# Kernel optimization log

Measured on AMD Instinct MI355X. Metric: run time of the kernel, lower is better.

The kernel has to match this reference:

```python
import jax, jax.numpy as jnp
import numpy as np

MAX_SEGMENTS = 196
BN_EPS = 1e-5

def _conv(x, w, pad, dil=1):
    return jax.lax.conv_general_dilated(
        x, w, window_strides=(1, 1), padding=[(pad, pad), (pad, pad)],
        rhs_dilation=(dil, dil), dimension_numbers=('NCHW', 'OIHW', 'NCHW'))

def _bn(x, g, b, m, v):
    inv = g / jnp.sqrt(v + BN_EPS)
    return x * inv[None, :, None, None] + (b - m * inv)[None, :, None, None]

def setup_inputs() -> dict:
    key = jax.random.key(0)
    ks = jax.random.split(key, 20)
    B, H, W = 2, 224, 224
    E = 768
    inp = {
        'img': jax.random.normal(ks[0], (B, 3, H, W), jnp.float32),
        'segments': jax.random.randint(ks[1], (B, H, W), 0, MAX_SEGMENTS, jnp.int32),
        'centroids': jax.random.uniform(ks[2], (B, MAX_SEGMENTS, 2), jnp.float32) * 223.0,
        'conv1_w': jax.random.normal(ks[3], (64, 3, 3, 3), jnp.float32) * 0.1,
        'conv1_b': jax.random.normal(ks[4], (64,), jnp.float32) * 0.1,
        'bn1_g': jax.random.uniform(ks[5], (64,), jnp.float32) + 0.5,
        'bn1_b': jax.random.normal(ks[6], (64,), jnp.float32) * 0.1,
        'bn1_m': jax.random.normal(ks[7], (64,), jnp.float32) * 0.1,
        'bn1_v': jax.random.uniform(ks[8], (64,), jnp.float32) + 0.5,
        'conv2_w': jax.random.normal(ks[9], (E, 64, 3, 3), jnp.float32) * 0.05,
        'conv2_b': jax.random.normal(ks[10], (E,), jnp.float32) * 0.1,
        'bn2_g': jax.random.uniform(ks[11], (E,), jnp.float32) + 0.5,
        'bn2_b': jax.random.normal(ks[12], (E,), jnp.float32) * 0.1,
        'bn2_m': jax.random.normal(ks[13], (E,), jnp.float32) * 0.1,
        'bn2_v': jax.random.uniform(ks[14], (E,), jnp.float32) + 0.5,
        'edge_w': jax.random.normal(ks[15], (2, 1, 3, 3), jnp.float32) * 0.2,
        'pos_w': jax.random.normal(ks[16], (E, 2), jnp.float32) * 0.5,
        'pos_b': jax.random.normal(ks[17], (E,), jnp.float32) * 0.1,
        'fusion_w': jax.random.normal(ks[18], (E, 2 * E), jnp.float32) * 0.02,
        'fusion_b': jax.random.normal(ks[19], (E,), jnp.float32) * 0.1,
    }
    return inp

def reference(img, segments, centroids, conv1_w, conv1_b, bn1_g, bn1_b, bn1_m, bn1_v,
              conv2_w, conv2_b, bn2_g, bn2_b, bn2_m, bn2_v, edge_w,
              pos_w, pos_b, fusion_w, fusion_b):
    B, _, H, W = img.shape
    M = MAX_SEGMENTS
    # CNN feature extractor: [B, E, H, W]
    x = jax.nn.relu(_bn(_conv(img, conv1_w, pad=1) + conv1_b[None, :, None, None],
                        bn1_g, bn1_b, bn1_m, bn1_v))
    feats = jax.nn.relu(_bn(_conv(x, conv2_w, pad=2, dil=2) + conv2_b[None, :, None, None],
                            bn2_g, bn2_b, bn2_m, bn2_v))
    C = feats.shape[1]
    # Edge detection on grayscale
    gray = jnp.mean(img, axis=1, keepdims=True)
    edges = _conv(gray, edge_w, pad=1)  # [B, 2, H, W]
    gradient_map = jnp.sqrt(edges[:, 0] ** 2 + edges[:, 1] ** 2 + 1e-8)  # [B, H, W]
    similarity = jnp.clip(1.0 - gradient_map, 0.0, 1.0)
    # Global per-(batch, segment) ids
    ids = (jnp.arange(B, dtype=jnp.int32)[:, None] * M + segments.reshape(B, -1)).reshape(-1)
    K = B * M
    ones = jnp.ones((B * H * W,), jnp.float32)
    counts = jax.ops.segment_sum(ones, ids, num_segments=K)              # [K]
    n_K = jnp.maximum(counts, 1.0)
    sim_sum = jax.ops.segment_sum(similarity.reshape(-1), ids, num_segments=K)
    W_k = (sim_sum / n_K).reshape(B, M)
    # Segment mean / max pooling of features
    ff = feats.transpose(0, 2, 3, 1).reshape(-1, C)                      # [B*H*W, C]
    emb_mean = (jax.ops.segment_sum(ff, ids, num_segments=K) / n_K[:, None]).reshape(B, M, C)
    mx = jax.ops.segment_max(ff, ids, num_segments=K)
    emb_max = jnp.where(counts[:, None] > 0, mx, 0.0).reshape(B, M, C)   # empty segments -> 0
    concat = jnp.concatenate([emb_mean, emb_max], axis=-1)               # [B, M, 2C]
    fused = jnp.einsum('bmc,dc->bmd', concat, fusion_w) + fusion_b
    weighted = fused * W_k[:, :, None]
    # Positional embeddings from normalized centroids
    cn = jnp.stack([centroids[:, :, 0] / float(W), centroids[:, :, 1] / float(H)], axis=-1)
    pos = jnp.einsum('bmc,dc->bmd', cn, pos_w) + pos_b                   # n_centroids == M
    final_embeddings = weighted + pos
    return final_embeddings, gradient_map, segments
```

## Files before the change

### kernel.cpp

```cpp
#include <hip/hip_runtime.h>
#include <hip/hip_fp8.h>

#define B_ 2
#define H_ 224
#define W_ 224
#define HW_ 50176
#define E_ 768
#define M_ 196

typedef __attribute__((ext_vector_type(8))) short short8;
typedef __attribute__((ext_vector_type(4))) float floatx4;

__device__ __forceinline__ float bf2f(ushort u){ return __uint_as_float(((unsigned)u)<<16); }
__device__ __forceinline__ ushort f2bf(float f){
  unsigned b = __float_as_uint(f);
  b += 0x7fffu + ((b>>16)&1u);
  return (ushort)(b>>16);
}
__device__ __forceinline__ unsigned pack4_fp8(float a, float b, float c, float d){
  int v = __builtin_amdgcn_cvt_pk_fp8_f32(a, b, 0, false);
  v = __builtin_amdgcn_cvt_pk_fp8_f32(c, d, v, true);
  return (unsigned)v;
}

__device__ __forceinline__ void ld_g2l16(const void* g, void* l){
  __builtin_amdgcn_global_load_lds((const __attribute__((address_space(1))) unsigned int*)g,
                                   (__attribute__((address_space(3))) unsigned int*)l, 16, 0, 0);
}

__global__ void prep_edge_k(const float* __restrict__ w2, const float* __restrict__ cb2,
                            const float* __restrict__ g2, const float* __restrict__ be2,
                            const float* __restrict__ mn2, const float* __restrict__ vr2,
                            ushort* __restrict__ wt2, float* __restrict__ bias2,
                            const float* __restrict__ w1, const float* __restrict__ cb1,
                            const float* __restrict__ g1, const float* __restrict__ be1,
                            const float* __restrict__ mn1, const float* __restrict__ vr1,
                            ushort* __restrict__ wA, float* __restrict__ bias1,
                            const float* __restrict__ img, const int* __restrict__ seg,
                            const float* __restrict__ ew, float* __restrict__ out,
                            float* __restrict__ counts, float* __restrict__ sims,
                            int* __restrict__ scnt){
  __shared__ ushort WT[9216];
  __shared__ float aux[196];
  __shared__ float aux2[196];
  int tid = threadIdx.x;
  if (blockIdx.x < 48){
    int co0 = blockIdx.x * 16;
    if (tid < 16){
      float inv = g2[co0+tid] * rsqrtf(vr2[co0+tid] + 1e-5f);
      aux[tid] = inv;
      bias2[co0+tid] = cb2[co0+tid]*inv + be2[co0+tid] - mn2[co0+tid]*inv;
    }
    __syncthreads();
    #pragma unroll
    for (int j = 0; j < 36; j++){
      int idx = j*256 + tid;
      WT[idx] = f2bf(w2[(size_t)co0*576 + idx] * aux[idx/576]);
    }
    __syncthreads();
    #pragma unroll
    for (int j = 0; j < 5; j++){
      int o = j*256 + tid;
      if (o < 1152){
        int tapkc = o >> 4, col = o & 15;
        int tap = tapkc >> 3, kc = tapkc & 7;
        ushort tmp[8];
        #pragma unroll
        for (int e=0; e<8; e++)
          tmp[e] = WT[col*576 + (kc*8+e)*9 + tap];
        *reinterpret_cast<uint4*>(&wt2[(size_t)((tap*8 + kc)*768 + co0 + col)*8]) =
            *reinterpret_cast<const uint4*>(tmp);
      }
    }
    return;
  }
  if (blockIdx.x == 48){
    #pragma unroll
    for (int j = 0; j < 8; j++){
      int t = j*256 + tid;
      int co = t >> 5, k = t & 31;
      float inv = g1[co] * rsqrtf(vr1[co] + 1e-5f);
      float val = 0.f;
      if (k < 27){
        int tap = k / 3, ci = k % 3;
        val = w1[co*27 + ci*9 + tap] * inv;
      }
      wA[co*32 + k] = f2bf(val);
      if (k == 0) bias1[co] = cb1[co]*inv + be1[co] - mn1[co]*inv;
    }
    return;
  }
  if (tid < 196){ aux[tid]=0.f; aux2[tid]=0.f; }
  __syncthreads();
  int p = (blockIdx.x-49)*256 + tid;
  int b = p / HW_; int r = p % HW_; int h = r / W_; int w = r % W_;
  float e0=0.f, e1=0.f;
  #pragma unroll
  for (int ky=0;ky<3;ky++){
    int hh=h+ky-1;
    #pragma unroll
    for (int kx=0;kx<3;kx++){
      int ww=w+kx-1;
      float gv=0.f;
      if (hh>=0&&hh<H_&&ww>=0&&ww<W_){
        int base = b*3*HW_ + hh*W_ + ww;
        gv=(img[base]+img[base+HW_]+img[base+2*HW_])*(1.f/3.f);
      }
      e0 += gv*ew[ky*3+kx];
      e1 += gv*ew[9+ky*3+kx];
    }
  }
  float gm = sqrtf(e0*e0+e1*e1+1e-8f);
  out[301056 + p] = gm;
  int sg = seg[p];
  out[401408 + p] = (float)sg;
  float sim = fminf(fmaxf(1.f-gm,0.f),1.f);
  atomicAdd(&aux[sg], 1.f);
  atomicAdd(&aux2[sg], sim);
  __syncthreads();
  if (tid < 196){
    int gid = b*196 + tid;
    float c = aux[tid];
    atomicAdd(&counts[gid], c);
    atomicAdd(&sims[gid], aux2[tid]);
    atomicAdd(&scnt[b*196+tid], (int)c);
  }
}

__launch_bounds__(256)
__global__ void conv1_scan_k(const float* __restrict__ img, const ushort* __restrict__ wA,
                             const float* __restrict__ bias1, ushort* __restrict__ xbf,
                             const int* __restrict__ scnt, int* __restrict__ offs,
                             int* __restrict__ curs){
  __shared__ float HL[3*18*20];
  __shared__ ushort IC[256*40];
  __shared__ ushort AW[64*40];
  __shared__ float b1s[64];
  int tid = threadIdx.x;
  if (blockIdx.x < 2){
    int* a = reinterpret_cast<int*>(HL);
    int s = blockIdx.x;
    a[tid] = (tid<196)? scnt[s*196+tid] : 0;
    __syncthreads();
    for (int d=1; d<256; d<<=1){
      int v = a[tid];
      int u = (tid>=d)? a[tid-d] : 0;
      __syncthreads();
      a[tid] = v+u;
      __syncthreads();
    }
    if (tid<=196) offs[s*200+tid] = tid ? a[tid-1] : 0;
    if (tid<196)  curs[s*196+tid] = tid ? a[tid-1] : 0;
    return;
  }
  int bid = blockIdx.x - 2;
  int b = bid / 196, tile = bid % 196;
  int tr = tile / 14, tc = tile % 14;
  int h0 = tr*16, w0 = tc*16;
  for (int idx = tid; idx < 972; idx += 256){
    int ci = idx / 324, rem = idx % 324;
    int r = rem / 18, c = rem % 18;
    int hh = h0 + r - 1, ww = w0 + c - 1;
    float v = (hh>=0 && hh<H_ && ww>=0 && ww<W_) ? img[((b*3+ci)*H_+hh)*W_+ww] : 0.f;
    HL[ci*360 + r*20 + c] = v;
  }
  {
    int row = tid >> 2, cp = (tid&3)*8;
    uint4 v = *reinterpret_cast<const uint4*>(&wA[row*32 + cp]);
    *reinterpret_cast<uint4*>(&AW[row*40 + cp]) = v;
  }
  if (tid < 64) b1s[tid] = bias1[tid];
  __syncthreads();
  {
    int pr = tid >> 4, pc = tid & 15;
    ushort tmp[32];
    #pragma unroll
    for (int ky=0; ky<3; ky++)
      #pragma unroll
      for (int kx=0; kx<3; kx++)
        #pragma unroll
        for (int ci=0; ci<3; ci++)
          tmp[(ky*3+kx)*3+ci] = f2bf(HL[ci*360 + (pr+ky)*20 + (pc+kx)]);
    #pragma unroll
    for (int k=27; k<32; k++) tmp[k] = 0;
    #pragma unroll
    for (int j=0; j<4; j++)
      *reinterpret_cast<uint4*>(&IC[tid*40 + j*8]) = *reinterpret_cast<const uint4*>(&tmp[j*8]);
  }
  __syncthreads();
  int lane = tid & 63, wave = tid >> 6;
  int q = lane >> 4, l15 = lane & 15;
  short8 af[4], bfr[4];
  #pragma unroll
  for (int f=0; f<4; f++)
    af[f] = *reinterpret_cast<const short8*>(&AW[(f*16+l15)*40 + q*8]);
  #pragma unroll
  for (int f=0; f<4; f++)
    bfr[f] = *reinterpret_cast<const short8*>(&IC[(wave*64+f*16+l15)*40 + q*8]);
  floatx4 acc[4][4];
  #pragma unroll
  for (int fc=0; fc<4; fc++)
    #pragma unroll
    for (int fp=0; fp<4; fp++){
      floatx4 z = (floatx4){0.f,0.f,0.f,0.f};
      acc[fc][fp] = __builtin_amdgcn_mfma_f32_16x16x32_bf16(af[fc], bfr[fp], z, 0,0,0);
    }
  #pragma unroll
  for (int fp=0; fp<4; fp++){
    int pxl = wave*64 + fp*16 + l15;
    size_t gp = (size_t)b*HW_ + (size_t)(h0 + (pxl>>4))*W_ + (w0 + (pxl&15));
    #pragma unroll
    for (int fc=0; fc<4; fc++){
      int co4 = fc*16 + q*4;
      ushort o[4];
      #pragma unroll
      for (int r=0; r<4; r++) o[r] = f2bf(fmaxf(acc[fc][fp][r] + b1s[co4+r], 0.f));
      *reinterpret_cast<uint2*>(&xbf[gp*64 + co4]) = *reinterpret_cast<const uint2*>(o);
    }
  }
}

__launch_bounds__(256, 2)
__global__ void conv2_scatter_k(const ushort* __restrict__ xbf, const ushort* __restrict__ wt2,
                                const float* __restrict__ bias2, unsigned char* __restrict__ feats,
                                const int* __restrict__ seg, int* __restrict__ curs,
                                int* __restrict__ list){
  __shared__ ushort SM[25600 + 12288];
  ushort* XH = SM;
  ushort* WL = SM + 25600;
  int tid = threadIdx.x;
  if (blockIdx.y == 0){
    if (blockIdx.x < 392){
      int p = blockIdx.x*256 + tid;
      int b = p / HW_;
      int pos = atomicAdd(&curs[b*196+seg[p]], 1);
      list[b*HW_ + pos] = p;
    }
    return;
  }
  int lane = tid & 63, wave = tid >> 6;
  int wc = wave >> 1, wp = wave & 1;
  int q = lane >> 4, l15 = lane & 15;
  int bt = blockIdx.x / 196, tile = blockIdx.x % 196;
  int tr = tile / 14, tc = tile % 14;
  int co0 = (blockIdx.y - 1) * 128;
  int h0 = tr*16, w0 = tc*16;

  for (int px = tid; px < 400; px += 256){
    int hr = px / 20, wcol = px % 20;
    int hh = h0 + hr - 2, ww = w0 + wcol - 2;
    bool ok = (hh>=0 && hh<H_ && ww>=0 && ww<W_);
    const uint4* src = reinterpret_cast<const uint4*>(&xbf[(((size_t)bt*H_+hh)*W_+ww)*64]);
    #pragma unroll
    for (int chl=0; chl<8; chl++){
      uint4 val = ok ? src[chl] : make_uint4(0u,0u,0u,0u);
      *reinterpret_cast<uint4*>(&XH[chl*3200 + px*8]) = val;
    }
  }
  #pragma unroll
  for (int j=0;j<4;j++){
    int idx = tid + 256*j;
    int srci = ((idx>>7)*768 + co0 + (idx&127))*8;
    ld_g2l16(&wt2[srci], &WL[(idx & ~63)*8]);
  }
  __syncthreads();

  floatx4 acc[4][8];
  #pragma unroll
  for (int i=0;i<4;i++)
    #pragma unroll
    for (int j=0;j<8;j++) acc[i][j] = (floatx4){0.f,0.f,0.f,0.f};

  int wbase = q*1024 + (wc*64 + l15)*8;
  int xb    = q*3200 + wp*1280 + l15*8;

  #pragma unroll
  for (int hs = 0; hs < 18; hs++){
    if (hs == 17) { asm volatile("s_waitcnt vmcnt(0)" ::: "memory"); }
    else          { asm volatile("s_waitcnt vmcnt(2)" ::: "memory"); }
    __builtin_amdgcn_s_barrier();
    const int s0 = (2*hs) % 6;
    if (hs < 16){
      const int p0 = (2*hs + 4) % 6;
      #pragma unroll
      for (int j=0;j<2;j++){
        int idx = tid + 256*j;
        int srci = ((4*(hs+2) + (idx>>7))*768 + co0 + (idx&127))*8;
        ld_g2l16(&wt2[srci], &WL[p0*2048 + (idx & ~63)*8]);
      }
    }
    const int tap = hs >> 1, half = hs & 1;
    const int dyr = (tap/3)*2, dxr = (tap%3)*2;
    const int xoff = half*12800 + dyr*160 + dxr*8;
    short8 af[4], bx[8];
    #pragma unroll
    for (int f=0; f<4; f++)
      af[f] = *reinterpret_cast<const short8*>(&WL[s0*2048 + wbase + f*128]);
    #pragma unroll
    for (int fp=0; fp<8; fp++)
      bx[fp] = *reinterpret_cast<const short8*>(&XH[xb + xoff + fp*160]);
    __builtin_amdgcn_s_setprio(1);
    #pragma unroll
    for (int fc=0; fc<4; fc++)
      #pragma unroll
      for (int fp=0; fp<8; fp++)
        acc[fc][fp] = __builtin_amdgcn_mfma_f32_16x16x32_bf16(af[fc], bx[fp], acc[fc][fp], 0,0,0);
    __builtin_amdgcn_s_setprio(0);
  }

  __syncthreads();
  unsigned* EP = reinterpret_cast<unsigned*>(SM);
  #pragma unroll
  for (int fc=0; fc<4; fc++){
    float4 bs = *reinterpret_cast<const float4*>(&bias2[co0 + wc*64 + fc*16 + q*4]);
    int cslot = wc*16 + fc*4 + q;
    #pragma unroll
    for (int fp=0; fp<8; fp++){
      int p_local = (wp*8 + fp)*16 + l15;
      EP[p_local*33 + cslot] = pack4_fp8(
          fmaxf(acc[fc][fp][0] + bs.x, 0.f), fmaxf(acc[fc][fp][1] + bs.y, 0.f),
          fmaxf(acc[fc][fp][2] + bs.z, 0.f), fmaxf(acc[fc][fp][3] + bs.w, 0.f));
    }
  }
  __syncthreads();
  {
    size_t gbase = ((size_t)bt*HW_ + (size_t)(tr*16)*W_ + tc*16)*768 + co0;
    int c = tid & 31, t5 = tid >> 5;
    #pragma unroll
    for (int j=0; j<32; j++){
      int px = j*8 + t5;
      int rr = px >> 4, wcol = px & 15;
      *reinterpret_cast<unsigned*>(
        &feats[gbase + ((size_t)rr*W_ + wcol)*768 + c*4]) = EP[px*33 + c];
    }
  }
}

__global__ void pool_k(const unsigned char* __restrict__ feats, const int* __restrict__ list,
                       const int* __restrict__ offs, float* __restrict__ meansum,
                       float* __restrict__ maxv){
  int m = blockIdx.x, qu = blockIdx.y, b = blockIdx.z, tid = threadIdx.x;
  int base = offs[b*200+m], end = offs[b*200+m+1];
  int len = end - base;
  int b0 = base + ((len*qu) >> 3);
  int b1 = base + ((len*(qu+1)) >> 3);
  const int* lp = &list[b*HW_];
  int co4 = tid*4;
  float s0=0.f,s1=0.f,s2=0.f,s3=0.f;
  float m0=0.f,m1=0.f,m2=0.f,m3=0.f;
  int i = b0;
  #define ACC(v) { \
    float f0=__builtin_amdgcn_cvt_f32_fp8((int)(v),0), f1=__builtin_amdgcn_cvt_f32_fp8((int)(v),1); \
    float f2=__builtin_amdgcn_cvt_f32_fp8((int)(v),2), f3=__builtin_amdgcn_cvt_f32_fp8((int)(v),3); \
    s0+=f0; s1+=f1; s2+=f2; s3+=f3; \
    m0=fmaxf(m0,f0); m1=fmaxf(m1,f1); m2=fmaxf(m2,f2); m3=fmaxf(m3,f3); }
  for (; i+3 < b1; i += 4){
    unsigned va = *reinterpret_cast<const unsigned*>(&feats[(size_t)lp[i  ]*768 + co4]);
    unsigned vb = *reinterpret_cast<const unsigned*>(&feats[(size_t)lp[i+1]*768 + co4]);
    unsigned vc = *reinterpret_cast<const unsigned*>(&feats[(size_t)lp[i+2]*768 + co4]);
    unsigned vd = *reinterpret_cast<const unsigned*>(&feats[(size_t)lp[i+3]*768 + co4]);
    ACC(va) ACC(vb) ACC(vc) ACC(vd)
  }
  for (; i < b1; i++){
    unsigned v = *reinterpret_cast<const unsigned*>(&feats[(size_t)lp[i]*768 + co4]);
    ACC(v)
  }
  #undef ACC
  int gs = b*196 + m;
  float* ms = &meansum[(size_t)gs*768 + co4];
  unsigned* mv = reinterpret_cast<unsigned*>(&maxv[(size_t)gs*768 + co4]);
  atomicAdd(&ms[0], s0); atomicAdd(&ms[1], s1);
  atomicAdd(&ms[2], s2); atomicAdd(&ms[3], s3);
  atomicMax(&mv[0], __float_as_uint(m0)); atomicMax(&mv[1], __float_as_uint(m1));
  atomicMax(&mv[2], __float_as_uint(m2)); atomicMax(&mv[3], __float_as_uint(m3));
}

__launch_bounds__(256)
__global__ void fusion_mfma_k(const float* __restrict__ meansum, const float* __restrict__ maxv,
                              const float* __restrict__ counts, const float* __restrict__ fw,
                              float* __restrict__ partial){
  __shared__ ushort SM2[2*128*72];
  ushort* AL = SM2;
  ushort* BL = SM2 + 128*72;
  int tid = threadIdx.x;
  int lane = tid & 63, wave = tid >> 6;
  int wc = wave >> 1, wp = wave & 1;
  int q = lane >> 4, l15 = lane & 15;
  int co0 = blockIdx.x * 128;
  int m0  = blockIdx.y * 128;
  int ksz = blockIdx.z;
  floatx4 acc[4][4];
  for (int i=0;i<4;i++) for (int j=0;j<4;j++) acc[i][j] = (floatx4){0.f,0.f,0.f,0.f};

  for (int kb=0; kb<3; kb++){
    int k0 = ksz*192 + kb*64;
    __syncthreads();
    #pragma unroll
    for (int i=0;i<4;i++){
      int idx = tid + 256*i;
      int row = idx >> 3, c8 = (idx & 7) * 8;
      int gm = m0 + row;
      float4 a0 = make_float4(0.f,0.f,0.f,0.f), a1 = a0;
      if (gm < 392){
        int k = k0 + c8;
        if (k < 768){
          float invc = 1.f / fmaxf(counts[gm], 1.f);
          a0 = *reinterpret_cast<const float4*>(&meansum[gm*768 + k]);
          a1 = *reinterpret_cast<const float4*>(&meansum[gm*768 + k + 4]);
          a0.x*=invc; a0.y*=invc; a0.z*=invc; a0.w*=invc;
          a1.x*=invc; a1.y*=invc; a1.z*=invc; a1.w*=invc;
        } else {
          a0 = *reinterpret_cast<const float4*>(&maxv[gm*768 + k - 768]);
          a1 = *reinterpret_cast<const float4*>(&maxv[gm*768 + k - 768 + 4]);
        }
      }
      ushort ua[8] = { f2bf(a0.x),f2bf(a0.y),f2bf(a0.z),f2bf(a0.w),
                       f2bf(a1.x),f2bf(a1.y),f2bf(a1.z),f2bf(a1.w) };
      *reinterpret_cast<uint4*>(&AL[row*72 + c8]) = *reinterpret_cast<uint4*>(ua);
      float4 b0 = *reinterpret_cast<const float4*>(&fw[(co0+row)*1536 + k0 + c8]);
      float4 b1 = *reinterpret_cast<const float4*>(&fw[(co0+row)*1536 + k0 + c8 + 4]);
      ushort ub[8] = { f2bf(b0.x),f2bf(b0.y),f2bf(b0.z),f2bf(b0.w),
                       f2bf(b1.x),f2bf(b1.y),f2bf(b1.z),f2bf(b1.w) };
      *reinterpret_cast<uint4*>(&BL[row*72 + c8]) = *reinterpret_cast<uint4*>(ub);
    }
    __syncthreads();
    #pragma unroll
    for (int ks=0; ks<64; ks+=32){
      short8 af[4], bfr[4];
      #pragma unroll
      for (int f=0; f<4; f++)
        af[f] = *reinterpret_cast<const short8*>(&AL[(wc*64+f*16+l15)*72 + ks + q*8]);
      #pragma unroll
      for (int f=0; f<4; f++)
        bfr[f] = *reinterpret_cast<const short8*>(&BL[(wp*64+f*16+l15)*72 + ks + q*8]);
      #pragma unroll
      for (int fm=0; fm<4; fm++)
        #pragma unroll
        for (int fn=0; fn<4; fn++)
          acc[fm][fn] = __builtin_amdgcn_mfma_f32_16x16x32_bf16(af[fm], bfr[fn], acc[fm][fn], 0,0,0);
    }
  }
  float* pp = &partial[(size_t)ksz * 301056];
  #pragma unroll
  for (int fm=0; fm<4; fm++){
    #pragma unroll
    for (int r2=0; r2<4; r2++){
      int m = m0 + wc*64 + fm*16 + q*4 + r2;
      if (m >= 392) continue;
      #pragma unroll
      for (int fn=0; fn<4; fn++){
        int co = co0 + wp*64 + fn*16 + l15;
        pp[(size_t)m*768 + co] = acc[fm][fn][r2];
      }
    }
  }
}

__global__ void fuse_ep_k(const float* __restrict__ partial, const float* __restrict__ fb,
                          const float* __restrict__ sims, const float* __restrict__ counts,
                          const float* __restrict__ cent, const float* __restrict__ pw,
                          const float* __restrict__ pb, float* __restrict__ out){
  int t = blockIdx.x*256 + threadIdx.x;
  int gm = t / 768, co = t % 768;
  float s = 0.f;
  #pragma unroll
  for (int k=0;k<8;k++) s += partial[(size_t)k*301056 + t];
  float wk = sims[gm] / fmaxf(counts[gm], 1.f);
  float cx = cent[gm*2 + 0] * (1.f/224.f);
  float cy = cent[gm*2 + 1] * (1.f/224.f);
  out[t] = (s + fb[co]) * wk + cx*pw[co*2] + cy*pw[co*2+1] + pb[co];
}

extern "C" void kernel_launch(void* const* d_in, const int* in_sizes, int n_in,
                              void* d_out, int out_size, void* d_ws, size_t ws_size,
                              hipStream_t stream){
  const float* img  = (const float*)d_in[0];
  const int*   seg  = (const int*)  d_in[1];
  const float* cent = (const float*)d_in[2];
  const float* c1w  = (const float*)d_in[3];
  const float* c1b  = (const float*)d_in[4];
  const float* bn1g = (const float*)d_in[5];
  const float* bn1b = (const float*)d_in[6];
  const float* bn1m = (const float*)d_in[7];
  const float* bn1v = (const float*)d_in[8];
  const float* c2w  = (const float*)d_in[9];
  const float* c2b  = (const float*)d_in[10];
  const float* bn2g = (const float*)d_in[11];
  const float* bn2b = (const float*)d_in[12];
  const float* bn2m = (const float*)d_in[13];
  const float* bn2v = (const float*)d_in[14];
  const float* ew   = (const float*)d_in[15];
  const float* pw   = (const float*)d_in[16];
  const float* pb   = (const float*)d_in[17];
  const float* fwp  = (const float*)d_in[18];
  const float* fbp  = (const float*)d_in[19];
  float* out = (float*)d_out;
  char* ws = (char*)d_ws;

  ushort* xbf    = (ushort*)(ws + 0);
  ushort* wt2    = (ushort*)(ws + 12845056);
  float*  bias2  = (float*) (ws + 13729792);
  float*  meansum= (float*) (ws + 13732864);
  float*  maxv   = (float*) (ws + 14937088);
  float*  counts = (float*) (ws + 16141312);
  float*  sims   = (float*) (ws + 16142880);
  int*    scnt   = (int*)   (ws + 16144448);
  int*    offs   = (int*)   (ws + 16147584);
  int*    curs   = (int*)   (ws + 16150784);
  int*    list   = (int*)   (ws + 16154112);
  ushort* wA     = (ushort*)(ws + 16154112);
  float*  bias1  = (float*) (ws + 16158208);
  unsigned char* feats = (unsigned char*)(ws + 16555520);
  float*  partial= (float*) (ws + 16555520);

  (void)hipMemsetAsync(ws + 13732864, 0, 2414720, stream);
  prep_edge_k<<<441, 256, 0, stream>>>(c2w, c2b, bn2g, bn2b, bn2m, bn2v, wt2, bias2,
                                       c1w, c1b, bn1g, bn1b, bn1m, bn1v, wA, bias1,
                                       img, seg, ew, out, counts, sims, scnt);
  conv1_scan_k<<<394, 256, 0, stream>>>(img, wA, bias1, xbf, scnt, offs, curs);
  conv2_scatter_k<<<dim3(392, 7), 256, 0, stream>>>(xbf, wt2, bias2, feats, seg, curs, list);
  pool_k<<<dim3(196, 8, 2), 192, 0, stream>>>(feats, list, offs, meansum, maxv);
  fusion_mfma_k<<<dim3(6, 4, 8), 256, 0, stream>>>(meansum, maxv, counts, fwp, partial);
  fuse_ep_k<<<1176, 256, 0, stream>>>(partial, fbp, sims, counts, cent, pw, pb, out);
}
```

Measured before the change: 306.9 us.

## Double-buffer LDS fragment loads in conv2 MFMA loop and repad epilogue

Restructures the conv2 main loop so the A/B fragments for the next half-step are read from LDS into a second register set while the current MFMAs run. The weight ring changes from six slots to three slots of double size with vmcnt(0) waits. The epilogue staging stride changes from 33 to 34 words. The aim is to hide LDS read latency behind MFMA work, at the cost of doubling fragment registers (which may lower occupancy) and a stricter wait on global loads.

```diff
diff --git a/kernel.cpp b/kernel.cpp
--- a/kernel.cpp
+++ b/kernel.cpp
@@ -258,10 +258,13 @@
     }
   }
   #pragma unroll
-  for (int j=0;j<4;j++){
-    int idx = tid + 256*j;
-    int srci = ((idx>>7)*768 + co0 + (idx&127))*8;
-    ld_g2l16(&wt2[srci], &WL[(idx & ~63)*8]);
+  for (int k=0;k<2;k++){
+    #pragma unroll
+    for (int j=0;j<2;j++){
+      int idx = tid + 256*j;
+      int srci = ((4*k + (idx>>7))*768 + co0 + (idx&127))*8;
+      ld_g2l16(&wt2[srci], &WL[k*4096 + (idx & ~63)*8]);
+    }
   }
   __syncthreads();
 
@@ -271,40 +274,49 @@
     #pragma unroll
     for (int j=0;j<8;j++) acc[i][j] = (floatx4){0.f,0.f,0.f,0.f};
 
-  int wbase = q*1024 + (wc*64 + l15)*8;
-  int xb    = q*3200 + wp*1280 + l15*8;
+  const int wbase = q*1024 + (wc*64 + l15)*8;
+  const int xb    = q*3200 + wp*1280 + l15*8;
+
+  short8 af[2][4], bx[2][8];
+  #pragma unroll
+  for (int f=0; f<4; f++)
+    af[0][f] = *reinterpret_cast<const short8*>(&WL[wbase + f*128]);
+  #pragma unroll
+  for (int fp=0; fp<8; fp++)
+    bx[0][fp] = *reinterpret_cast<const short8*>(&XH[xb + fp*160]);
 
   #pragma unroll
   for (int hs = 0; hs < 18; hs++){
-    if (hs == 17) { asm volatile("s_waitcnt vmcnt(0)" ::: "memory"); }
-    else          { asm volatile("s_waitcnt vmcnt(2)" ::: "memory"); }
-    __builtin_amdgcn_s_barrier();
-    const int s0 = (2*hs) % 6;
+    const int cur = hs & 1, nxt = cur ^ 1;
+    asm volatile("s_waitcnt vmcnt(0)\n\ts_barrier" ::: "memory");
     if (hs < 16){
-      const int p0 = (2*hs + 4) % 6;
       #pragma unroll
       for (int j=0;j<2;j++){
         int idx = tid + 256*j;
         int srci = ((4*(hs+2) + (idx>>7))*768 + co0 + (idx&127))*8;
-        ld_g2l16(&wt2[srci], &WL[p0*2048 + (idx & ~63)*8]);
+        ld_g2l16(&wt2[srci], &WL[((hs+2)%3)*4096 + (idx & ~63)*8]);
       }
     }
-    const int tap = hs >> 1, half = hs & 1;
-    const int dyr = (tap/3)*2, dxr = (tap%3)*2;
-    const int xoff = half*12800 + dyr*160 + dxr*8;
-    short8 af[4], bx[8];
-    #pragma unroll
-    for (int f=0; f<4; f++)
-      af[f] = *reinterpret_cast<const short8*>(&WL[s0*2048 + wbase + f*128]);
-    #pragma unroll
-    for (int fp=0; fp<8; fp++)
-      bx[fp] = *reinterpret_cast<const short8*>(&XH[xb + xoff + fp*160]);
+    if (hs < 17){
+      const int nh = hs + 1;
+      const int ntap = nh >> 1, nhalf = nh & 1;
+      const int ndyr = (ntap/3)*2, ndxr = (ntap%3)*2;
+      const int nxoff = nhalf*12800 + ndyr*160 + ndxr*8;
+      const int nring = (nh % 3) * 4096;
+      #pragma unroll
+      for (int f=0; f<4; f++)
+        af[nxt][f] = *reinterpret_cast<const short8*>(&WL[nring + wbase + f*128]);
+      #pragma unroll
+      for (int fp=0; fp<8; fp++)
+        bx[nxt][fp] = *reinterpret_cast<const short8*>(&XH[xb + nxoff + fp*160]);
+    }
     __builtin_amdgcn_s_setprio(1);
     #pragma unroll
     for (int fc=0; fc<4; fc++)
       #pragma unroll
       for (int fp=0; fp<8; fp++)
-        acc[fc][fp] = __builtin_amdgcn_mfma_f32_16x16x32_bf16(af[fc], bx[fp], acc[fc][fp], 0,0,0);
+        acc[fc][fp] = __builtin_amdgcn_mfma_f32_16x16x32_bf16(af[cur][fc], bx[cur][fp],
+                                                              acc[fc][fp], 0,0,0);
     __builtin_amdgcn_s_setprio(0);
   }
 
@@ -317,7 +329,7 @@
     #pragma unroll
     for (int fp=0; fp<8; fp++){
       int p_local = (wp*8 + fp)*16 + l15;
-      EP[p_local*33 + cslot] = pack4_fp8(
+      EP[p_local*34 + cslot] = pack4_fp8(
           fmaxf(acc[fc][fp][0] + bs.x, 0.f), fmaxf(acc[fc][fp][1] + bs.y, 0.f),
           fmaxf(acc[fc][fp][2] + bs.z, 0.f), fmaxf(acc[fc][fp][3] + bs.w, 0.f));
     }
@@ -331,7 +343,7 @@
       int px = j*8 + t5;
       int rr = px >> 4, wcol = px & 15;
       *reinterpret_cast<unsigned*>(
-        &feats[gbase + ((size_t)rr*W_ + wcol)*768 + c*4]) = EP[px*33 + c];
+        &feats[gbase + ((size_t)rr*W_ + wcol)*768 + c*4]) = EP[px*34 + c];
     }
   }
 }
```

Measured after the change: 307.0 us. Within noise of the previous version (+0.0%).

## Load conv2 weight fragments directly into registers with double buffering, drop LDS staging

Applied to the files above, without the earlier changes.

The conv2 MFMA loop no longer stages weights through LDS with async global-to-LDS loads and per-step barriers. Each wave now loads its own weight fragments from global memory straight into registers, prefetching the next step's fragments one iteration ahead, and the per-iteration barrier is removed. This shrinks LDS use, which may allow more resident blocks and reduces synchronisation. The cost is duplicated global/L2 weight traffic across the two pixel waves and exposed global latency if one step of prefetch is not enough. The epilogue LDS stride also changes from 33 to 34.

```diff
diff --git a/kernel.cpp b/kernel.cpp
--- a/kernel.cpp
+++ b/kernel.cpp
@@ -21,11 +21,6 @@
   int v = __builtin_amdgcn_cvt_pk_fp8_f32(a, b, 0, false);
   v = __builtin_amdgcn_cvt_pk_fp8_f32(c, d, v, true);
   return (unsigned)v;
-}
-
-__device__ __forceinline__ void ld_g2l16(const void* g, void* l){
-  __builtin_amdgcn_global_load_lds((const __attribute__((address_space(1))) unsigned int*)g,
-                                   (__attribute__((address_space(3))) unsigned int*)l, 16, 0, 0);
 }
 
 __global__ void prep_edge_k(const float* __restrict__ w2, const float* __restrict__ cb2,
@@ -225,9 +220,8 @@
                                 const float* __restrict__ bias2, unsigned char* __restrict__ feats,
                                 const int* __restrict__ seg, int* __restrict__ curs,
                                 int* __restrict__ list){
-  __shared__ ushort SM[25600 + 12288];
+  __shared__ ushort SM[25600];
   ushort* XH = SM;
-  ushort* WL = SM + 25600;
   int tid = threadIdx.x;
   if (blockIdx.y == 0){
     if (blockIdx.x < 392){
@@ -257,12 +251,6 @@
       *reinterpret_cast<uint4*>(&XH[chl*3200 + px*8]) = val;
     }
   }
-  #pragma unroll
-  for (int j=0;j<4;j++){
-    int idx = tid + 256*j;
-    int srci = ((idx>>7)*768 + co0 + (idx&127))*8;
-    ld_g2l16(&wt2[srci], &WL[(idx & ~63)*8]);
-  }
   __syncthreads();
 
   floatx4 acc[4][8];
@@ -271,40 +259,37 @@
     #pragma unroll
     for (int j=0;j<8;j++) acc[i][j] = (floatx4){0.f,0.f,0.f,0.f};
 
-  int wbase = q*1024 + (wc*64 + l15)*8;
-  int xb    = q*3200 + wp*1280 + l15*8;
+  const int xb = q*3200 + wp*1280 + l15*8;
+  const ushort* wgl = wt2 + ((size_t)q*768 + (size_t)(co0 + wc*64 + l15))*8;
+
+  short8 af[2][4];
+  #pragma unroll
+  for (int f=0; f<4; f++)
+    af[0][f] = *reinterpret_cast<const short8*>(&wgl[f*128]);
 
   #pragma unroll
   for (int hs = 0; hs < 18; hs++){
-    if (hs == 17) { asm volatile("s_waitcnt vmcnt(0)" ::: "memory"); }
-    else          { asm volatile("s_waitcnt vmcnt(2)" ::: "memory"); }
-    __builtin_amdgcn_s_barrier();
-    const int s0 = (2*hs) % 6;
-    if (hs < 16){
-      const int p0 = (2*hs + 4) % 6;
-      #pragma unroll
-      for (int j=0;j<2;j++){
-        int idx = tid + 256*j;
-        int srci = ((4*(hs+2) + (idx>>7))*768 + co0 + (idx&127))*8;
-        ld_g2l16(&wt2[srci], &WL[p0*2048 + (idx & ~63)*8]);
-      }
-    }
+    const int cur = hs & 1, nxt = cur ^ 1;
     const int tap = hs >> 1, half = hs & 1;
     const int dyr = (tap/3)*2, dxr = (tap%3)*2;
     const int xoff = half*12800 + dyr*160 + dxr*8;
-    short8 af[4], bx[8];
-    #pragma unroll
-    for (int f=0; f<4; f++)
-      af[f] = *reinterpret_cast<const short8*>(&WL[s0*2048 + wbase + f*128]);
+    short8 bx[8];
     #pragma unroll
     for (int fp=0; fp<8; fp++)
       bx[fp] = *reinterpret_cast<const short8*>(&XH[xb + xoff + fp*160]);
+    if (hs < 17){
+      #pragma unroll
+      for (int f=0; f<4; f++)
+        af[nxt][f] = *reinterpret_cast<const short8*>(&wgl[(size_t)(hs+1)*24576 + f*128]);
+    }
+    __builtin_amdgcn_sched_barrier(0);
     __builtin_amdgcn_s_setprio(1);
     #pragma unroll
     for (int fc=0; fc<4; fc++)
       #pragma unroll
       for (int fp=0; fp<8; fp++)
-        acc[fc][fp] = __builtin_amdgcn_mfma_f32_16x16x32_bf16(af[fc], bx[fp], acc[fc][fp], 0,0,0);
+        acc[fc][fp] = __builtin_amdgcn_mfma_f32_16x16x32_bf16(af[cur][fc], bx[fp],
+                                                              acc[fc][fp], 0,0,0);
     __builtin_amdgcn_s_setprio(0);
   }
 
@@ -317,7 +302,7 @@
     #pragma unroll
     for (int fp=0; fp<8; fp++){
       int p_local = (wp*8 + fp)*16 + l15;
-      EP[p_local*33 + cslot] = pack4_fp8(
+      EP[p_local*34 + cslot] = pack4_fp8(
           fmaxf(acc[fc][fp][0] + bs.x, 0.f), fmaxf(acc[fc][fp][1] + bs.y, 0.f),
           fmaxf(acc[fc][fp][2] + bs.z, 0.f), fmaxf(acc[fc][fp][3] + bs.w, 0.f));
     }
@@ -331,7 +316,7 @@
       int px = j*8 + t5;
       int rr = px >> 4, wcol = px & 15;
       *reinterpret_cast<unsigned*>(
-        &feats[gbase + ((size_t)rr*W_ + wcol)*768 + c*4]) = EP[px*33 + c];
+        &feats[gbase + ((size_t)rr*W_ + wcol)*768 + c*4]) = EP[px*34 + c];
     }
   }
 }
```

Result: faster. 300.5 us (-2.1%).
